# Kernel optimization log

Hardware: AMD Instinct MI355X
Metric: run time of the kernel (lower is better)

Reference implementation:

```python
import jax, jax.numpy as jnp
import numpy as np

EPS = 1e-12  # torch f.normalize eps


def _rms_norm(x, g):
    # f.normalize(x, dim=1) * g * sqrt(C): L2-normalize over channel dim
    c = x.shape[1]
    n = jnp.maximum(jnp.linalg.norm(x, axis=1, keepdims=True), EPS)
    return x / n * g * (c ** 0.5)


def setup_inputs() -> dict:
    key = jax.random.key(0)
    ks = jax.random.split(key, 5)
    b, dim, H, W = 32, 256, 64, 64
    heads, dim_head, num_mem = 4, 32, 4
    hidden = heads * dim_head
    return {
        "x": jax.random.normal(ks[0], (b, dim, H, W), dtype=jnp.float32),
        "g1": jnp.ones((1, dim, 1, 1), dtype=jnp.float32),
        "mem_kv": jax.random.normal(ks[1], (2, heads, dim_head, num_mem), dtype=jnp.float32),
        "w_qkv": jax.random.normal(ks[2], (3 * hidden, dim), dtype=jnp.float32) * (1.0 / np.sqrt(dim)),
        "w_out": jax.random.normal(ks[3], (dim, hidden), dtype=jnp.float32) * (1.0 / np.sqrt(hidden)),
        "b_out": jnp.zeros((dim,), dtype=jnp.float32),
        "g2": jnp.ones((1, dim, 1, 1), dtype=jnp.float32),
    }


def reference(x, g1, mem_kv, w_qkv, w_out, b_out, g2):
    b, c, H, W = x.shape
    _, heads, dim_head, num_mem = mem_kv.shape
    n = H * W
    scale = dim_head ** -0.5

    xn = _rms_norm(x, g1)
    # 1x1 conv qkv projection: [b, 3*hidden, H, W]
    qkv = jnp.einsum('oc,bchw->bohw', w_qkv, xn)
    hidden = heads * dim_head
    q, k, v = jnp.split(qkv, 3, axis=1)
    # b (h d) x y -> b h d (x y)
    q = q.reshape(b, heads, dim_head, n)
    k = k.reshape(b, heads, dim_head, n)
    v = v.reshape(b, heads, dim_head, n)

    mk = jnp.broadcast_to(mem_kv[0], (b, heads, dim_head, num_mem))
    mv = jnp.broadcast_to(mem_kv[1], (b, heads, dim_head, num_mem))
    k = jnp.concatenate([mk, k], axis=-1)
    v = jnp.concatenate([mv, v], axis=-1)

    q = jax.nn.softmax(q, axis=-2) * scale  # softmax over head dim d
    k = jax.nn.softmax(k, axis=-1)          # softmax over sequence n

    context = jnp.einsum('bhdn,bhen->bhde', k, v)   # [b,h,d,e]
    out = jnp.einsum('bhde,bhdn->bhen', context, q)  # [b,h,e,n]
    out = out.reshape(b, hidden, H, W)

    o = jnp.einsum('oc,bchw->bohw', w_out, out) + b_out[None, :, None, None]
    return _rms_norm(o, g2)
```

## Files before the change

kernel.cpp:

```cpp
#include <hip/hip_runtime.h>
#include <math.h>

#define CC   256
#define HW   4096
#define OC3  384
#define HID  128
#define DH   32
#define NM   4
#define NPART 8
#define SCALE 0.17677669529663688f

typedef __bf16 bf16x8 __attribute__((ext_vector_type(8)));
typedef float  f32x4  __attribute__((ext_vector_type(4)));

__device__ __forceinline__ ushort f2bf(float x) {
    union { float f; unsigned u; } v; v.f = x;
    unsigned r = v.u + 0x7fffu + ((v.u >> 16) & 1u);
    return (ushort)(r >> 16);
}
__device__ __forceinline__ float bf2f(ushort b) {
    union { unsigned u; float f; } v; v.u = ((unsigned)b) << 16; return v.f;
}
__device__ __forceinline__ void g2l16(const void* g, void* l) {
    __builtin_amdgcn_global_load_lds(
        (const __attribute__((address_space(1))) void*)g,
        (__attribute__((address_space(3))) void*)l, 16, 0, 0);
}

__global__ __launch_bounds__(256) void k_xn(const float* __restrict__ x,
        const float* __restrict__ wqkv, const float* __restrict__ g1,
        const float* __restrict__ wout,
        ushort* __restrict__ wq2t, ushort* __restrict__ woutt,
        ushort* __restrict__ xnT) {
    __shared__ float xt[256 * 36];
    __shared__ float ps[8 * 33];
    __shared__ float invn[32];
    int tid = threadIdx.x;
    if (blockIdx.x < 384) {
        int o = blockIdx.x;
        wq2t[(size_t)o * CC + tid] = f2bf(wqkv[(size_t)o * CC + tid] * g1[tid] * 16.0f);
        if (o < CC && tid < HID) woutt[(size_t)o * HID + tid] = f2bf(wout[(size_t)o * HID + tid]);
    }
    int pix0 = blockIdx.x * 32;
    int b = pix0 >> 12, hw0 = pix0 & 4095;
    int p = tid & 31, cg = tid >> 5;
    const float* xb = x + (size_t)b * CC * HW + hw0;
    {
        int cr = tid >> 3;
        int chunk = tid & 7;
        #pragma unroll
        for (int pass = 0; pass < 8; ++pass) {
            int c = pass * 32 + cr;
            float4 v = *(const float4*)&xb[(size_t)c * HW + chunk * 4];
            *(float4*)&xt[c * 36 + chunk * 4] = v;
        }
    }
    __syncthreads();
    float s = 0.f;
    #pragma unroll 8
    for (int i = 0; i < 32; ++i) { float v = xt[(cg * 32 + i) * 36 + p]; s += v * v; }
    ps[cg * 33 + p] = s;
    __syncthreads();
    if (tid < 32) {
        float t = 0.f;
        #pragma unroll
        for (int g = 0; g < 8; ++g) t += ps[g * 33 + tid];
        invn[tid] = 1.0f / fmaxf(sqrtf(t), 1e-12f);
    }
    __syncthreads();
    float inv = invn[p];
    ushort* dst = xnT + ((size_t)(pix0 + p)) * CC + cg * 32;
    #pragma unroll
    for (int q = 0; q < 4; ++q) {
        uint4 pk; ushort* o8 = (ushort*)&pk;
        #pragma unroll
        for (int i = 0; i < 8; ++i) o8[i] = f2bf(xt[(cg * 32 + q * 8 + i) * 36 + p] * inv);
        *(uint4*)&dst[q * 8] = pk;
    }
}

__global__ __launch_bounds__(256) void k_qkv(const ushort* __restrict__ wq2t,
        const ushort* __restrict__ xnT, ushort* __restrict__ qkv) {
    __shared__ __align__(16) ushort As[2][128 * 32];
    __shared__ __align__(16) ushort Bs[2][128 * 32];
    int tid = threadIdx.x;
    int lin = blockIdx.x + 2 * (blockIdx.y + 32 * blockIdx.z);
    int swz = (lin & 7) * 256 + (lin >> 3);
    int m0 = 128 + (swz % 2) * 128;
    int t_ = swz / 2;
    int p0 = (t_ & 31) * 128;
    int b  = t_ >> 5;
    int lane = tid & 63, wid = tid >> 6;
    int l15 = tid & 15, quad = (tid >> 4) & 3;
    int wm = wid >> 1, wn = wid & 1;
    int rsub = lane >> 2;
    const ushort* Ab = wq2t + (size_t)m0 * CC;
    const ushort* Bb = xnT + ((size_t)(b * HW + p0)) * CC;
    f32x4 acc[4][4];
    #pragma unroll
    for (int i = 0; i < 4; ++i)
        #pragma unroll
        for (int j = 0; j < 4; ++j) acc[i][j] = (f32x4){0.f, 0.f, 0.f, 0.f};

    auto stage = [&](int buf, int k0) {
        #pragma unroll
        for (int q = 0; q < 2; ++q) {
            int rw = wid * 32 + q * 16;
            int r  = rw + rsub;
            int sc = (lane & 3) ^ ((r >> 1) & 3);
            g2l16(Ab + (size_t)r * CC + k0 + sc * 8, &As[buf][rw * 32]);
            g2l16(Bb + (size_t)r * CC + k0 + sc * 8, &Bs[buf][rw * 32]);
        }
    };

    stage(0, 0);
    __syncthreads();
    #pragma unroll
    for (int s = 0; s < 8; ++s) {
        int cur = s & 1;
        if (s < 7) stage(cur ^ 1, (s + 1) * 32);
        bf16x8 af[4], bfr[4];
        #pragma unroll
        for (int mt = 0; mt < 4; ++mt) {
            int ra = wm * 64 + mt * 16 + l15;
            af[mt] = *(const bf16x8*)&As[cur][ra * 32 + ((quad ^ ((ra >> 1) & 3)) << 3)];
        }
        #pragma unroll
        for (int nt = 0; nt < 4; ++nt) {
            int rb = wn * 64 + nt * 16 + l15;
            bfr[nt] = *(const bf16x8*)&Bs[cur][rb * 32 + ((quad ^ ((rb >> 1) & 3)) << 3)];
        }
        #pragma unroll
        for (int mt = 0; mt < 4; ++mt)
            #pragma unroll
            for (int nt = 0; nt < 4; ++nt)
                acc[mt][nt] = __builtin_amdgcn_mfma_f32_16x16x32_bf16(
                                  af[mt], bfr[nt], acc[mt][nt], 0, 0, 0);
        __syncthreads();
    }
    #pragma unroll
    for (int mt = 0; mt < 4; ++mt) {
        int o = m0 + wm * 64 + mt * 16 + quad * 4;
        #pragma unroll
        for (int nt = 0; nt < 4; ++nt) {
            int pix = p0 + wn * 64 + nt * 16 + l15;
            ushort* dst = qkv + ((size_t)(b * OC3 + o)) * HW + pix;
            #pragma unroll
            for (int r = 0; r < 4; ++r) dst[(size_t)r * HW] = f2bf(acc[mt][nt][r]);
        }
    }
}

__global__ __launch_bounds__(256) void k_ctx(const ushort* __restrict__ qkv,
        float* __restrict__ ctxp, float* __restrict__ mstat, float* __restrict__ sstat) {
    __shared__ __align__(16) char smem[32768];
    ushort* klw = (ushort*)smem;
    ushort* vlw = (ushort*)(smem + 16384);
    float*  red = (float*)smem;
    __shared__ float mred[4][32];
    __shared__ float sred[4][32];
    int tid = threadIdx.x;
    int lane = tid & 63, wid = tid >> 6;
    int l15 = lane & 15, quad = lane >> 4;
    int bh = blockIdx.x, part = blockIdx.y;
    int b = bh >> 2, h = bh & 3;
    int r  = lane >> 1;
    int ch = (lane & 1) * 32;
    const ushort* kp = qkv + ((size_t)(b * OC3 + HID + h * DH) + r) * HW + part * 512;
    const ushort* vp = qkv + ((size_t)(b * OC3 + 2 * HID + h * DH) + r) * HW + part * 512;
    ushort* myk = klw + wid * 2048;
    ushort* myv = vlw + wid * 2048;

    uint4 kreg[2][4];
    float lm = -1e30f;
    #pragma unroll
    for (int t = 0; t < 2; ++t) {
        int n0 = wid * 64 + t * 256;
        #pragma unroll
        for (int i = 0; i < 4; ++i) {
            kreg[t][i] = *(const uint4*)&kp[n0 + ch + i * 8];
            const ushort* ke = (const ushort*)&kreg[t][i];
            #pragma unroll
            for (int j = 0; j < 8; ++j) lm = fmaxf(lm, bf2f(ke[j]));
        }
    }
    lm = fmaxf(lm, __shfl_xor(lm, 1));
    if ((lane & 1) == 0) mred[wid][r] = lm;
    __syncthreads();
    float mp = fmaxf(fmaxf(mred[0][r], mred[1][r]), fmaxf(mred[2][r], mred[3][r]));

    f32x4 acc[2][2];
    #pragma unroll
    for (int i = 0; i < 2; ++i)
        #pragma unroll
        for (int j = 0; j < 2; ++j) acc[i][j] = (f32x4){0.f, 0.f, 0.f, 0.f};
    float ls = 0.f;
    #pragma unroll
    for (int t = 0; t < 2; ++t) {
        int n0 = wid * 64 + t * 256;
        #pragma unroll
        for (int i = 0; i < 4; ++i) {
            uint4 vv4 = *(const uint4*)&vp[n0 + ch + i * 8];
            uint4 ko; ushort* kw = (ushort*)&ko; const ushort* ke = (const ushort*)&kreg[t][i];
            #pragma unroll
            for (int j = 0; j < 8; ++j) {
                float e = __expf(bf2f(ke[j]) - mp);
                ls += e;
                kw[j] = f2bf(e);
            }
            int boff = ((ch + i * 8) * 2) ^ ((r & 7) << 4);
            *(uint4*)((char*)&myk[r * 64] + boff) = ko;
            *(uint4*)((char*)&myv[r * 64] + boff) = vv4;
        }
        #pragma unroll
        for (int ks = 0; ks < 2; ++ks) {
            bf16x8 af[2], bf[2];
            #pragma unroll
            for (int dt = 0; dt < 2; ++dt) {
                int row = dt * 16 + l15;
                int boff = (ks * 64 + quad * 16) ^ ((row & 7) << 4);
                af[dt] = *(const bf16x8*)((char*)&myk[row * 64] + boff);
                bf[dt] = *(const bf16x8*)((char*)&myv[row * 64] + boff);
            }
            #pragma unroll
            for (int dt = 0; dt < 2; ++dt)
                #pragma unroll
                for (int et = 0; et < 2; ++et)
                    acc[dt][et] = __builtin_amdgcn_mfma_f32_16x16x32_bf16(
                                      af[dt], bf[et], acc[dt][et], 0, 0, 0);
        }
    }
    ls += __shfl_xor(ls, 1);
    if ((lane & 1) == 0) sred[wid][r] = ls;
    __syncthreads();
    if (tid < 32) {
        float s = sred[0][tid] + sred[1][tid] + sred[2][tid] + sred[3][tid];
        float m2 = fmaxf(fmaxf(mred[0][tid], mred[1][tid]),
                         fmaxf(mred[2][tid], mred[3][tid]));
        size_t o = ((size_t)part * 128 + bh) * 32 + tid;
        mstat[o] = m2;
        sstat[o] = s;
    }
    #pragma unroll
    for (int dt = 0; dt < 2; ++dt)
        #pragma unroll
        for (int et = 0; et < 2; ++et)
            #pragma unroll
            for (int rr = 0; rr < 4; ++rr) {
                int d = dt * 16 + quad * 4 + rr;
                int e = et * 16 + l15;
                red[wid * 1024 + d * 32 + e] = acc[dt][et][rr];
            }
    __syncthreads();
    {
        int o0 = tid * 4;
        f32x4 s4 = (f32x4){0.f, 0.f, 0.f, 0.f};
        #pragma unroll
        for (int w = 0; w < 4; ++w) {
            f32x4 v = *(const f32x4*)&red[w * 1024 + o0];
            s4[0] += v[0]; s4[1] += v[1]; s4[2] += v[2]; s4[3] += v[3];
        }
        *(f32x4*)&ctxp[(size_t)part * 131072 + (size_t)bh * 1024 + o0] = s4;
    }
}

__global__ __launch_bounds__(256) void k_w2(const float* __restrict__ ctxp,
        const float* __restrict__ mstat, const float* __restrict__ sstat,
        const float* __restrict__ memkv,
        const ushort* __restrict__ woutt, ushort* __restrict__ W2) {
    __shared__ ushort ctxb[4 * 32 * 40];
    __shared__ float scl[NPART][128];
    __shared__ float memsc[128][NM];
    int tid = threadIdx.x, b = blockIdx.x;
    int wid = tid >> 6;
    int l15 = tid & 15, quad = (tid >> 4) & 3;
    if (tid < 128) {
        int h = tid >> 5, d = tid & 31;
        size_t base = (size_t)(b * 4 + h) * 32 + d;
        float mp[NPART];
        float M = -1e30f;
        #pragma unroll
        for (int p = 0; p < NPART; ++p) { mp[p] = mstat[(size_t)p * 4096 + base]; M = fmaxf(M, mp[p]); }
        float mk[NM];
        #pragma unroll
        for (int m = 0; m < NM; ++m) { mk[m] = memkv[(h * DH + d) * NM + m]; M = fmaxf(M, mk[m]); }
        float Z = 0.f;
        #pragma unroll
        for (int p = 0; p < NPART; ++p) Z += sstat[(size_t)p * 4096 + base] * __expf(mp[p] - M);
        #pragma unroll
        for (int m = 0; m < NM; ++m) Z += __expf(mk[m] - M);
        float iz = 1.0f / Z;
        #pragma unroll
        for (int p = 0; p < NPART; ++p) scl[p][tid] = __expf(mp[p] - M) * iz;
        #pragma unroll
        for (int m = 0; m < NM; ++m) memsc[tid][m] = __expf(mk[m] - M) * iz;
    }
    __syncthreads();
    #pragma unroll
    for (int j = 0; j < 16; ++j) {
        int idx = tid + j * 256;
        int rr = idx >> 5;
        int e  = idx & 31;
        int h  = idx >> 10, d = (idx >> 5) & 31;
        float s = 0.f;
        #pragma unroll
        for (int p = 0; p < NPART; ++p)
            s += ctxp[(size_t)p * 131072 + (size_t)b * 4096 + idx] * scl[p][rr];
        #pragma unroll
        for (int m = 0; m < NM; ++m)
            s += memsc[rr][m] * memkv[512 + (h * DH + e) * NM + m];
        ctxb[(h * 32 + d) * 40 + e] = f2bf(s);
    }
    __syncthreads();
    #pragma unroll
    for (int h = 0; h < 4; ++h) {
        f32x4 acc[4][2];
        #pragma unroll
        for (int i = 0; i < 4; ++i)
            #pragma unroll
            for (int j = 0; j < 2; ++j) acc[i][j] = (f32x4){0.f, 0.f, 0.f, 0.f};
        bf16x8 af[4], bfr[2];
        #pragma unroll
        for (int mt = 0; mt < 4; ++mt)
            af[mt] = *(const bf16x8*)&woutt[(size_t)(wid * 64 + mt * 16 + l15) * HID
                                            + h * DH + quad * 8];
        #pragma unroll
        for (int nt = 0; nt < 2; ++nt)
            bfr[nt] = *(const bf16x8*)&ctxb[(h * 32 + nt * 16 + l15) * 40 + quad * 8];
        #pragma unroll
        for (int mt = 0; mt < 4; ++mt)
            #pragma unroll
            for (int nt = 0; nt < 2; ++nt)
                acc[mt][nt] = __builtin_amdgcn_mfma_f32_16x16x32_bf16(
                                  af[mt], bfr[nt], acc[mt][nt], 0, 0, 0);
        #pragma unroll
        for (int mt = 0; mt < 4; ++mt)
            #pragma unroll
            for (int nt = 0; nt < 2; ++nt)
                #pragma unroll
                for (int r = 0; r < 4; ++r) {
                    int oc = wid * 64 + mt * 16 + quad * 4 + r;
                    int d  = nt * 16 + l15;
                    W2[((size_t)b * CC + oc) * HID + h * DH + d] = f2bf(acc[mt][nt][r]);
                }
    }
}

__global__ __launch_bounds__(256) void k_final(const ushort* __restrict__ xnT,
        const ushort* __restrict__ wq2t, const ushort* __restrict__ W2,
        const float* __restrict__ bout, const float* __restrict__ g2,
        float* __restrict__ y) {
    __shared__ __align__(16) char smem[52224];
    ushort* xnTs = (ushort*)smem;
    float*  red  = (float*)smem;
    float*  invs = (float*)(smem + 4352);
    ushort* Qw   = (ushort*)(smem + 16384);
    ushort* sq   = (ushort*)(smem + 32768);
    float*  bl   = (float*)(smem + 50176);
    float*  gl   = (float*)(smem + 51200);
    int tid = threadIdx.x;
    int b = blockIdx.y;
    int hwb = blockIdx.x * 64;
    int lane = tid & 63, wid = tid >> 6;
    int l15 = tid & 15, quad = (tid >> 4) & 3;
    int rsub = lane >> 2;
    bl[tid] = bout[tid];
    gl[tid] = g2[tid];

    auto stageX = [&](int half) {
        const ushort* xb = xnT + ((size_t)(b * HW + hwb)) * CC + half * 128;
        #pragma unroll
        for (int qq = 0; qq < 4; ++qq) {
            int r0 = qq * 16 + wid * 4;
            int r  = r0 + (lane >> 4);
            int g  = (lane & 15) ^ (r & 7);
            g2l16(xb + (size_t)r * CC + g * 8, &xnTs[r0 * 128]);
        }
    };
    auto stageQ = [&](int buf, int k0) {
        #pragma unroll
        for (int qq = 0; qq < 2; ++qq) {
            int rw = wid * 32 + qq * 16;
            int r  = rw + rsub;
            int sc = (lane & 3) ^ ((r >> 1) & 3);
            g2l16(wq2t + (size_t)r * CC + k0 + sc * 8, &Qw[buf * 4096 + rw * 32]);
        }
    };

    f32x4 accq[2][4];
    #pragma unroll
    for (int i = 0; i < 2; ++i)
        #pragma unroll
        for (int j = 0; j < 4; ++j) accq[i][j] = (f32x4){0.f, 0.f, 0.f, 0.f};
    stageX(0);
    stageQ(0, 0);
    __syncthreads();
    #pragma unroll
    for (int s = 0; s < 8; ++s) {
        int cur = s & 1;
        if (s < 7 && s != 3) stageQ(cur ^ 1, (s + 1) * 32);
        bf16x8 af[2], bfr[4];
        #pragma unroll
        for (int mt = 0; mt < 2; ++mt) {
            int ra = wid * 32 + mt * 16 + l15;
            af[mt] = *(const bf16x8*)&Qw[cur * 4096 + ra * 32 + ((quad ^ ((ra >> 1) & 3)) << 3)];
        }
        int cread = (s & 3) * 4 + quad;
        #pragma unroll
        for (int nt = 0; nt < 4; ++nt) {
            int rb = nt * 16 + l15;
            bfr[nt] = *(const bf16x8*)&xnTs[rb * 128 + ((cread ^ (rb & 7)) << 3)];
        }
        #pragma unroll
        for (int mt = 0; mt < 2; ++mt)
            #pragma unroll
            for (int nt = 0; nt < 4; ++nt)
                accq[mt][nt] = __builtin_amdgcn_mfma_f32_16x16x32_bf16(
                                   af[mt], bfr[nt], accq[mt][nt], 0, 0, 0);
        if (s == 3) {
            __syncthreads();
            stageX(1);
            stageQ(cur ^ 1, 128);
        }
        __syncthreads();
    }

    #pragma unroll
    for (int nt = 0; nt < 4; ++nt) {
        float m = -1e30f;
        #pragma unroll
        for (int mt = 0; mt < 2; ++mt)
            #pragma unroll
            for (int r = 0; r < 4; ++r) m = fmaxf(m, accq[mt][nt][r]);
        m = fmaxf(m, __shfl_xor(m, 16));
        m = fmaxf(m, __shfl_xor(m, 32));
        float s = 0.f;
        float e[2][4];
        #pragma unroll
        for (int mt = 0; mt < 2; ++mt)
            #pragma unroll
            for (int r = 0; r < 4; ++r) { e[mt][r] = __expf(accq[mt][nt][r] - m); s += e[mt][r]; }
        s += __shfl_xor(s, 16);
        s += __shfl_xor(s, 32);
        float r_ = SCALE / s;
        int pix = nt * 16 + l15;
        #pragma unroll
        for (int mt = 0; mt < 2; ++mt)
            #pragma unroll
            for (int r = 0; r < 4; ++r)
                sq[pix * 136 + wid * 32 + mt * 16 + quad * 4 + r] = f2bf(e[mt][r] * r_);
    }

    ushort* WsQ = Qw;
    f32x4 acc[4][4];
    #pragma unroll
    for (int i = 0; i < 4; ++i)
        #pragma unroll
        for (int j = 0; j < 4; ++j) acc[i][j] = (f32x4){0.f, 0.f, 0.f, 0.f};
    const ushort* W2b = W2 + (size_t)b * CC * HID;
    for (int k0 = 0; k0 < HID; k0 += 32) {
        __syncthreads();
        #pragma unroll
        for (int q = 0; q < 4; ++q) {
            int rw = wid * 64 + q * 16;
            int r  = rw + rsub;
            int sc = (lane & 3) ^ ((r >> 1) & 3);
            g2l16(W2b + (size_t)r * HID + k0 + sc * 8, &WsQ[rw * 32]);
        }
        __syncthreads();
        bf16x8 af[4], bfr[4];
        #pragma unroll
        for (int mt = 0; mt < 4; ++mt) {
            int ra = wid * 64 + mt * 16 + l15;
            af[mt] = *(const bf16x8*)&WsQ[ra * 32 + ((quad ^ ((ra >> 1) & 3)) << 3)];
        }
        #pragma unroll
        for (int nt = 0; nt < 4; ++nt)
            bfr[nt] = *(const bf16x8*)&sq[(nt * 16 + l15) * 136 + k0 + quad * 8];
        #pragma unroll
        for (int mt = 0; mt < 4; ++mt)
            #pragma unroll
            for (int nt = 0; nt < 4; ++nt)
                acc[mt][nt] = __builtin_amdgcn_mfma_f32_16x16x32_bf16(
                                  af[mt], bfr[nt], acc[mt][nt], 0, 0, 0);
    }

    float part[4] = {0.f, 0.f, 0.f, 0.f};
    #pragma unroll
    for (int mt = 0; mt < 4; ++mt)
        #pragma unroll
        for (int r = 0; r < 4; ++r) {
            int oc = wid * 64 + mt * 16 + quad * 4 + r;
            float bo = bl[oc];
            #pragma unroll
            for (int nt = 0; nt < 4; ++nt) {
                float v = acc[mt][nt][r] + bo;
                acc[mt][nt][r] = v;
                part[nt] += v * v;
            }
        }
    __syncthreads();
    #pragma unroll
    for (int nt = 0; nt < 4; ++nt)
        red[(nt * 16 + l15) * 17 + wid * 4 + quad] = part[nt];
    __syncthreads();
    if (tid < 64) {
        float s = 0.f;
        #pragma unroll
        for (int g = 0; g < 16; ++g) s += red[tid * 17 + g];
        invs[tid] = 1.0f / fmaxf(sqrtf(s), 1e-12f);
    }
    __syncthreads();
    #pragma unroll
    for (int mt = 0; mt < 4; ++mt)
        #pragma unroll
        for (int nt = 0; nt < 4; ++nt) {
            int pix = nt * 16 + l15;
            float iv = invs[pix];
            #pragma unroll
            for (int r = 0; r < 4; ++r) {
                int oc = wid * 64 + mt * 16 + quad * 4 + r;
                y[((size_t)(b * CC + oc)) * HW + hwb + pix] = acc[mt][nt][r] * iv * gl[oc] * 16.0f;
            }
        }
}

extern "C" void kernel_launch(void* const* d_in, const int* in_sizes, int n_in,
                              void* d_out, int out_size, void* d_ws, size_t ws_size,
                              hipStream_t stream) {
    const float* x     = (const float*)d_in[0];
    const float* g1    = (const float*)d_in[1];
    const float* memkv = (const float*)d_in[2];
    const float* wqkv  = (const float*)d_in[3];
    const float* wout  = (const float*)d_in[4];
    const float* bout  = (const float*)d_in[5];
    const float* g2    = (const float*)d_in[6];
    float* y = (float*)d_out;

    char* w = (char*)d_ws;
    ushort* wq2t  = (ushort*)w;  w += (size_t)OC3 * CC * 2;
    ushort* woutt = (ushort*)w;  w += (size_t)CC * HID * 2;
    float*  mstat = (float*)w;   w += (size_t)NPART * 4096 * 4;
    float*  sstat = (float*)w;   w += (size_t)NPART * 4096 * 4;
    float*  ctxp  = (float*)w;   w += (size_t)NPART * 131072 * 4;
    ushort* W2    = (ushort*)w;  w += (size_t)32 * CC * HID * 2;
    ushort* xnT   = (ushort*)w;  w += (size_t)32 * HW * CC * 2;
    ushort* qkv   = (ushort*)w;  w += (size_t)32 * OC3 * HW * 2;

    k_xn    <<<dim3(4096),      dim3(256), 0, stream>>>(x, wqkv, g1, wout, wq2t, woutt, xnT);
    k_qkv   <<<dim3(2, 32, 32), dim3(256), 0, stream>>>(wq2t, xnT, qkv);
    k_ctx   <<<dim3(128, 8),    dim3(256), 0, stream>>>(qkv, ctxp, mstat, sstat);
    k_w2    <<<dim3(32),        dim3(256), 0, stream>>>(ctxp, mstat, sstat, memkv, woutt, W2);
    k_final <<<dim3(64, 32),    dim3(256), 0, stream>>>(xnT, wq2t, W2, bout, g2, y);
}
```

Baseline: 344.0 us.

## Fuse K/V projection GEMM with context accumulation, skipping qkv round-trip

Replaces the separate qkv projection kernel and context kernel with one kernel that computes K and V tiles for 128 pixels in registers, applies the per-tile softmax max/exp on K, stages bf16 K/V tiles in shared memory and computes partial context products per head. This removes writing and re-reading the K/V activations through global memory and one kernel launch. The partition count grows from 8 to 32, so more partial context and stat buffers are written and then reduced in k_w2. Context compute is split across waves in two sequential phases, which leaves some waves idle.

```diff
diff --git a/kernel.cpp b/kernel.cpp
--- a/kernel.cpp
+++ b/kernel.cpp
@@ -7,7 +7,7 @@
 #define HID  128
 #define DH   32
 #define NM   4
-#define NPART 8
+#define NPART 32
 #define SCALE 0.17677669529663688f
 
 typedef __bf16 bf16x8 __attribute__((ext_vector_type(8)));
@@ -79,28 +79,33 @@
     }
 }
 
-__global__ __launch_bounds__(256) void k_qkv(const ushort* __restrict__ wq2t,
-        const ushort* __restrict__ xnT, ushort* __restrict__ qkv) {
-    __shared__ __align__(16) ushort As[2][128 * 32];
-    __shared__ __align__(16) ushort Bs[2][128 * 32];
+__global__ __launch_bounds__(256) void k_kv(const ushort* __restrict__ wq2t,
+        const ushort* __restrict__ xnT, float* __restrict__ ctxp,
+        float* __restrict__ mstat, float* __restrict__ sstat) {
+    __shared__ __align__(16) char smem[51200];
+    ushort* AsK = (ushort*)smem;
+    ushort* AsV = (ushort*)(smem + 16384);
+    ushort* BsB = (ushort*)(smem + 32768);
+    ushort* ktile = (ushort*)smem;
+    ushort* vtile = (ushort*)(smem + 16384);
+    float* mred = (float*)(smem + 49152);
+    float* sred = (float*)(smem + 50176);
     int tid = threadIdx.x;
-    int lin = blockIdx.x + 2 * (blockIdx.y + 32 * blockIdx.z);
-    int swz = (lin & 7) * 256 + (lin >> 3);
-    int m0 = 128 + (swz % 2) * 128;
-    int t_ = swz / 2;
-    int p0 = (t_ & 31) * 128;
-    int b  = t_ >> 5;
     int lane = tid & 63, wid = tid >> 6;
     int l15 = tid & 15, quad = (tid >> 4) & 3;
     int wm = wid >> 1, wn = wid & 1;
     int rsub = lane >> 2;
-    const ushort* Ab = wq2t + (size_t)m0 * CC;
+    int part = blockIdx.x & 31;
+    int b    = blockIdx.x >> 5;
+    int p0 = part * 128;
+    const ushort* Ak = wq2t + (size_t)HID * CC;
+    const ushort* Av = wq2t + (size_t)(2 * HID) * CC;
     const ushort* Bb = xnT + ((size_t)(b * HW + p0)) * CC;
-    f32x4 acc[4][4];
+    f32x4 ak[4][4], av[4][4];
     #pragma unroll
     for (int i = 0; i < 4; ++i)
         #pragma unroll
-        for (int j = 0; j < 4; ++j) acc[i][j] = (f32x4){0.f, 0.f, 0.f, 0.f};
+        for (int j = 0; j < 4; ++j) { ak[i][j] = (f32x4){0,0,0,0}; av[i][j] = (f32x4){0,0,0,0}; }
 
     auto stage = [&](int buf, int k0) {
         #pragma unroll
@@ -108,8 +113,9 @@
             int rw = wid * 32 + q * 16;
             int r  = rw + rsub;
             int sc = (lane & 3) ^ ((r >> 1) & 3);
-            g2l16(Ab + (size_t)r * CC + k0 + sc * 8, &As[buf][rw * 32]);
-            g2l16(Bb + (size_t)r * CC + k0 + sc * 8, &Bs[buf][rw * 32]);
+            g2l16(Ak + (size_t)r * CC + k0 + sc * 8, &AsK[buf * 4096 + rw * 32]);
+            g2l16(Av + (size_t)r * CC + k0 + sc * 8, &AsV[buf * 4096 + rw * 32]);
+            g2l16(Bb + (size_t)r * CC + k0 + sc * 8, &BsB[buf * 4096 + rw * 32]);
         }
     };
 
@@ -119,149 +125,145 @@
     for (int s = 0; s < 8; ++s) {
         int cur = s & 1;
         if (s < 7) stage(cur ^ 1, (s + 1) * 32);
-        bf16x8 af[4], bfr[4];
+        bf16x8 afk[4], afv[4], bfr[4];
         #pragma unroll
         for (int mt = 0; mt < 4; ++mt) {
             int ra = wm * 64 + mt * 16 + l15;
-            af[mt] = *(const bf16x8*)&As[cur][ra * 32 + ((quad ^ ((ra >> 1) & 3)) << 3)];
+            int off = cur * 4096 + ra * 32 + ((quad ^ ((ra >> 1) & 3)) << 3);
+            afk[mt] = *(const bf16x8*)&AsK[off];
+            afv[mt] = *(const bf16x8*)&AsV[off];
         }
         #pragma unroll
         for (int nt = 0; nt < 4; ++nt) {
             int rb = wn * 64 + nt * 16 + l15;
-            bfr[nt] = *(const bf16x8*)&Bs[cur][rb * 32 + ((quad ^ ((rb >> 1) & 3)) << 3)];
-        }
+            bfr[nt] = *(const bf16x8*)&BsB[cur * 4096 + rb * 32 + ((quad ^ ((rb >> 1) & 3)) << 3)];
+        }
+        #pragma unroll
+        for (int mt = 0; mt < 4; ++mt)
+            #pragma unroll
+            for (int nt = 0; nt < 4; ++nt) {
+                ak[mt][nt] = __builtin_amdgcn_mfma_f32_16x16x32_bf16(afk[mt], bfr[nt], ak[mt][nt], 0, 0, 0);
+                av[mt][nt] = __builtin_amdgcn_mfma_f32_16x16x32_bf16(afv[mt], bfr[nt], av[mt][nt], 0, 0, 0);
+            }
+        __syncthreads();
+    }
+
+    float mloc[4][4];
+    #pragma unroll
+    for (int mt = 0; mt < 4; ++mt)
+        #pragma unroll
+        for (int r = 0; r < 4; ++r) {
+            float m = ak[mt][0][r];
+            #pragma unroll
+            for (int nt = 1; nt < 4; ++nt) m = fmaxf(m, ak[mt][nt][r]);
+            #pragma unroll
+            for (int sh = 1; sh < 16; sh <<= 1) m = fmaxf(m, __shfl_xor(m, sh));
+            mloc[mt][r] = m;
+        }
+    if (l15 == 0)
+        #pragma unroll
+        for (int mt = 0; mt < 4; ++mt)
+            #pragma unroll
+            for (int r = 0; r < 4; ++r)
+                mred[wn * 128 + wm * 64 + mt * 16 + quad * 4 + r] = mloc[mt][r];
+    __syncthreads();
+
+    #pragma unroll
+    for (int mt = 0; mt < 4; ++mt)
+        #pragma unroll
+        for (int r = 0; r < 4; ++r) {
+            int o = wm * 64 + mt * 16 + quad * 4 + r;
+            float mp = fmaxf(mred[o], mred[128 + o]);
+            float sl = 0.f;
+            #pragma unroll
+            for (int nt = 0; nt < 4; ++nt) {
+                float e = __expf(ak[mt][nt][r] - mp);
+                ak[mt][nt][r] = e;
+                sl += e;
+            }
+            #pragma unroll
+            for (int sh = 1; sh < 16; sh <<= 1) sl += __shfl_xor(sl, sh);
+            if (l15 == 0) sred[wn * 128 + o] = sl;
+        }
+    if (wm == 0) {
         #pragma unroll
         for (int mt = 0; mt < 4; ++mt)
             #pragma unroll
             for (int nt = 0; nt < 4; ++nt)
-                acc[mt][nt] = __builtin_amdgcn_mfma_f32_16x16x32_bf16(
-                                  af[mt], bfr[nt], acc[mt][nt], 0, 0, 0);
-        __syncthreads();
-    }
-    #pragma unroll
-    for (int mt = 0; mt < 4; ++mt) {
-        int o = m0 + wm * 64 + mt * 16 + quad * 4;
-        #pragma unroll
-        for (int nt = 0; nt < 4; ++nt) {
-            int pix = p0 + wn * 64 + nt * 16 + l15;
-            ushort* dst = qkv + ((size_t)(b * OC3 + o)) * HW + pix;
-            #pragma unroll
-            for (int r = 0; r < 4; ++r) dst[(size_t)r * HW] = f2bf(acc[mt][nt][r]);
-        }
-    }
-}
-
-__global__ __launch_bounds__(256) void k_ctx(const ushort* __restrict__ qkv,
-        float* __restrict__ ctxp, float* __restrict__ mstat, float* __restrict__ sstat) {
-    __shared__ __align__(16) char smem[32768];
-    ushort* klw = (ushort*)smem;
-    ushort* vlw = (ushort*)(smem + 16384);
-    float*  red = (float*)smem;
-    __shared__ float mred[4][32];
-    __shared__ float sred[4][32];
-    int tid = threadIdx.x;
-    int lane = tid & 63, wid = tid >> 6;
-    int l15 = lane & 15, quad = lane >> 4;
-    int bh = blockIdx.x, part = blockIdx.y;
-    int b = bh >> 2, h = bh & 3;
-    int r  = lane >> 1;
-    int ch = (lane & 1) * 32;
-    const ushort* kp = qkv + ((size_t)(b * OC3 + HID + h * DH) + r) * HW + part * 512;
-    const ushort* vp = qkv + ((size_t)(b * OC3 + 2 * HID + h * DH) + r) * HW + part * 512;
-    ushort* myk = klw + wid * 2048;
-    ushort* myv = vlw + wid * 2048;
-
-    uint4 kreg[2][4];
-    float lm = -1e30f;
-    #pragma unroll
-    for (int t = 0; t < 2; ++t) {
-        int n0 = wid * 64 + t * 256;
-        #pragma unroll
-        for (int i = 0; i < 4; ++i) {
-            kreg[t][i] = *(const uint4*)&kp[n0 + ch + i * 8];
-            const ushort* ke = (const ushort*)&kreg[t][i];
-            #pragma unroll
-            for (int j = 0; j < 8; ++j) lm = fmaxf(lm, bf2f(ke[j]));
-        }
-    }
-    lm = fmaxf(lm, __shfl_xor(lm, 1));
-    if ((lane & 1) == 0) mred[wid][r] = lm;
-    __syncthreads();
-    float mp = fmaxf(fmaxf(mred[0][r], mred[1][r]), fmaxf(mred[2][r], mred[3][r]));
-
-    f32x4 acc[2][2];
-    #pragma unroll
-    for (int i = 0; i < 2; ++i)
-        #pragma unroll
-        for (int j = 0; j < 2; ++j) acc[i][j] = (f32x4){0.f, 0.f, 0.f, 0.f};
-    float ls = 0.f;
-    #pragma unroll
-    for (int t = 0; t < 2; ++t) {
-        int n0 = wid * 64 + t * 256;
-        #pragma unroll
-        for (int i = 0; i < 4; ++i) {
-            uint4 vv4 = *(const uint4*)&vp[n0 + ch + i * 8];
-            uint4 ko; ushort* kw = (ushort*)&ko; const ushort* ke = (const ushort*)&kreg[t][i];
-            #pragma unroll
-            for (int j = 0; j < 8; ++j) {
-                float e = __expf(bf2f(ke[j]) - mp);
-                ls += e;
-                kw[j] = f2bf(e);
-            }
-            int boff = ((ch + i * 8) * 2) ^ ((r & 7) << 4);
-            *(uint4*)((char*)&myk[r * 64] + boff) = ko;
-            *(uint4*)((char*)&myv[r * 64] + boff) = vv4;
-        }
-        #pragma unroll
-        for (int ks = 0; ks < 2; ++ks) {
-            bf16x8 af[2], bf[2];
+                #pragma unroll
+                for (int r = 0; r < 4; ++r) {
+                    int row = mt * 16 + quad * 4 + r;
+                    int pix = wn * 64 + nt * 16 + l15;
+                    int boff = (row * 256 + pix * 2) ^ ((row & 7) << 4);
+                    *(ushort*)((char*)ktile + boff) = f2bf(ak[mt][nt][r]);
+                    *(ushort*)((char*)vtile + boff) = f2bf(av[mt][nt][r]);
+                }
+    }
+    __syncthreads();
+
+    if (tid < 128) {
+        float m2 = fmaxf(mred[tid], mred[128 + tid]);
+        float s2 = sred[tid] + sred[128 + tid];
+        int h = tid >> 5, d = tid & 31;
+        size_t o = ((size_t)part * 128 + (b * 4 + h)) * 32 + d;
+        mstat[o] = m2;
+        sstat[o] = s2;
+    }
+    auto ctxPhase = [&](int hl, int h) {
+        f32x4 c2[2][2];
+        #pragma unroll
+        for (int i = 0; i < 2; ++i)
+            #pragma unroll
+            for (int j = 0; j < 2; ++j) c2[i][j] = (f32x4){0,0,0,0};
+        #pragma unroll
+        for (int ks = 0; ks < 4; ++ks) {
+            bf16x8 a2[2], b2[2];
             #pragma unroll
             for (int dt = 0; dt < 2; ++dt) {
-                int row = dt * 16 + l15;
-                int boff = (ks * 64 + quad * 16) ^ ((row & 7) << 4);
-                af[dt] = *(const bf16x8*)((char*)&myk[row * 64] + boff);
-                bf[dt] = *(const bf16x8*)((char*)&myv[row * 64] + boff);
+                int row = hl * 32 + dt * 16 + l15;
+                int boff = (row * 256 + (ks * 32 + quad * 8) * 2) ^ ((row & 7) << 4);
+                a2[dt] = *(const bf16x8*)((char*)ktile + boff);
+                b2[dt] = *(const bf16x8*)((char*)vtile + boff);
             }
             #pragma unroll
             for (int dt = 0; dt < 2; ++dt)
                 #pragma unroll
                 for (int et = 0; et < 2; ++et)
-                    acc[dt][et] = __builtin_amdgcn_mfma_f32_16x16x32_bf16(
-                                      af[dt], bf[et], acc[dt][et], 0, 0, 0);
-        }
-    }
-    ls += __shfl_xor(ls, 1);
-    if ((lane & 1) == 0) sred[wid][r] = ls;
-    __syncthreads();
-    if (tid < 32) {
-        float s = sred[0][tid] + sred[1][tid] + sred[2][tid] + sred[3][tid];
-        float m2 = fmaxf(fmaxf(mred[0][tid], mred[1][tid]),
-                         fmaxf(mred[2][tid], mred[3][tid]));
-        size_t o = ((size_t)part * 128 + bh) * 32 + tid;
-        mstat[o] = m2;
-        sstat[o] = s;
-    }
-    #pragma unroll
-    for (int dt = 0; dt < 2; ++dt)
-        #pragma unroll
-        for (int et = 0; et < 2; ++et)
-            #pragma unroll
-            for (int rr = 0; rr < 4; ++rr) {
-                int d = dt * 16 + quad * 4 + rr;
-                int e = et * 16 + l15;
-                red[wid * 1024 + d * 32 + e] = acc[dt][et][rr];
-            }
-    __syncthreads();
-    {
-        int o0 = tid * 4;
-        f32x4 s4 = (f32x4){0.f, 0.f, 0.f, 0.f};
-        #pragma unroll
-        for (int w = 0; w < 4; ++w) {
-            f32x4 v = *(const f32x4*)&red[w * 1024 + o0];
-            s4[0] += v[0]; s4[1] += v[1]; s4[2] += v[2]; s4[3] += v[3];
-        }
-        *(f32x4*)&ctxp[(size_t)part * 131072 + (size_t)bh * 1024 + o0] = s4;
-    }
+                    c2[dt][et] = __builtin_amdgcn_mfma_f32_16x16x32_bf16(a2[dt], b2[et], c2[dt][et], 0, 0, 0);
+        }
+        float* dst = ctxp + ((size_t)part * 128 + (b * 4 + h)) * 1024;
+        #pragma unroll
+        for (int dt = 0; dt < 2; ++dt)
+            #pragma unroll
+            for (int et = 0; et < 2; ++et)
+                #pragma unroll
+                for (int rr = 0; rr < 4; ++rr) {
+                    int d = dt * 16 + quad * 4 + rr;
+                    int e = et * 16 + l15;
+                    dst[d * 32 + e] = c2[dt][et][rr];
+                }
+    };
+    if (wid == 0) ctxPhase(0, 0);
+    if (wid == 1) ctxPhase(1, 1);
+    __syncthreads();
+
+    if (wm == 1) {
+        #pragma unroll
+        for (int mt = 0; mt < 4; ++mt)
+            #pragma unroll
+            for (int nt = 0; nt < 4; ++nt)
+                #pragma unroll
+                for (int r = 0; r < 4; ++r) {
+                    int row = mt * 16 + quad * 4 + r;
+                    int pix = wn * 64 + nt * 16 + l15;
+                    int boff = (row * 256 + pix * 2) ^ ((row & 7) << 4);
+                    *(ushort*)((char*)ktile + boff) = f2bf(ak[mt][nt][r]);
+                    *(ushort*)((char*)vtile + boff) = f2bf(av[mt][nt][r]);
+                }
+    }
+    __syncthreads();
+    if (wid == 2) ctxPhase(0, 2);
+    if (wid == 3) ctxPhase(1, 3);
 }
 
 __global__ __launch_bounds__(256) void k_w2(const float* __restrict__ ctxp,
@@ -277,8 +279,8 @@
     if (tid < 128) {
         int h = tid >> 5, d = tid & 31;
         size_t base = (size_t)(b * 4 + h) * 32 + d;
+        float M = -1e30f;
         float mp[NPART];
-        float M = -1e30f;
         #pragma unroll
         for (int p = 0; p < NPART; ++p) { mp[p] = mstat[(size_t)p * 4096 + base]; M = fmaxf(M, mp[p]); }
         float mk[NM];
@@ -545,11 +547,9 @@
     float*  ctxp  = (float*)w;   w += (size_t)NPART * 131072 * 4;
     ushort* W2    = (ushort*)w;  w += (size_t)32 * CC * HID * 2;
     ushort* xnT   = (ushort*)w;  w += (size_t)32 * HW * CC * 2;
-    ushort* qkv   = (ushort*)w;  w += (size_t)32 * OC3 * HW * 2;
 
     k_xn    <<<dim3(4096),      dim3(256), 0, stream>>>(x, wqkv, g1, wout, wq2t, woutt, xnT);
-    k_qkv   <<<dim3(2, 32, 32), dim3(256), 0, stream>>>(wq2t, xnT, qkv);
-    k_ctx   <<<dim3(128, 8),    dim3(256), 0, stream>>>(qkv, ctxp, mstat, sstat);
+    k_kv    <<<dim3(1024),      dim3(256), 0, stream>>>(wq2t, xnT, ctxp, mstat, sstat);
     k_w2    <<<dim3(32),        dim3(256), 0, stream>>>(ctxp, mstat, sstat, memkv, woutt, W2);
     k_final <<<dim3(64, 32),    dim3(256), 0, stream>>>(xnT, wq2t, W2, bout, g2, y);
 }
```

New measurement: 444.8 us. +29.3%, slower.
